# Performance work log

Hardware: AMD Instinct MI355X
Metric: run time of the kernel (lower is better)

The kernel has to match this reference:

```python
import jax, jax.numpy as jnp
import numpy as np

N, K, E = 50000, 32, 50000 * 32
IN_DIM, FEAT_DIM, HID_DIM, OUT_DIM = 128, 64, 64, 32
EPS = 1e-12  # F.normalize eps


def setup_inputs() -> dict:
    key = jax.random.key(0)
    ks = jax.random.split(key, 16)
    s = 0.1  # small init scale (stand-in for xavier)
    return {
        "feat": jax.random.normal(ks[0], (N, IN_DIM), jnp.float32),
        "dists_max": jax.random.uniform(ks[1], (N, K), jnp.float32),
        "src": jax.random.randint(ks[2], (E,), 0, N, jnp.int32),
        "dst": jax.random.randint(ks[3], (E,), 0, N, jnp.int32),
        "w_pre": jax.random.normal(ks[4], (FEAT_DIM, IN_DIM), jnp.float32) * s,
        "b_pre": jnp.zeros((FEAT_DIM,), jnp.float32),
        "Wu1": jax.random.normal(ks[5], (HID_DIM, FEAT_DIM), jnp.float32) * s,
        "bu1": jnp.zeros((HID_DIM,), jnp.float32),
        "Wv1": jax.random.normal(ks[6], (HID_DIM, FEAT_DIM), jnp.float32) * s,
        "bv1": jnp.zeros((HID_DIM,), jnp.float32),
        "wp1": jax.random.normal(ks[7], (1, HID_DIM), jnp.float32) * s,
        "bp1": jnp.zeros((1,), jnp.float32),
        "Wu2": jax.random.normal(ks[8], (OUT_DIM, HID_DIM), jnp.float32) * s,
        "bu2": jnp.zeros((OUT_DIM,), jnp.float32),
        "Wv2": jax.random.normal(ks[9], (OUT_DIM, HID_DIM), jnp.float32) * s,
        "bv2": jnp.zeros((OUT_DIM,), jnp.float32),
        "wp2": jax.random.normal(ks[10], (1, OUT_DIM), jnp.float32) * s,
        "bp2": jnp.zeros((1,), jnp.float32),
    }


def _pgnn_layer(x, sp_dist, src, dst, Wu, bu, Wv, bv, wp, bp, n, k):
    # x: [N, Din]; sp_dist: [E]; src/dst: [E] (anchor edges, E = N*K)
    u = x @ Wu.T + bu  # [N, D]
    v = x @ Wv.T + bv  # [N, D]
    # u_mul_e then v_add_e: message = v_feat[dst] + u_feat[src] * sp_dist
    msg = v[dst] + u[src] * sp_dist[:, None]          # [E, D]
    msg = jax.nn.relu(msg).reshape(n, k, -1)          # [N, K, D]
    out_position = (msg @ wp.T + bp)[..., 0]          # [N, K]
    out_structure = jnp.mean(msg, axis=1)             # [N, D]
    return out_position, out_structure


def reference(feat, dists_max, src, dst, w_pre, b_pre,
              Wu1, bu1, Wv1, bv1, wp1, bp1,
              Wu2, bu2, Wv2, bv2, wp2, bp2):
    n, k = dists_max.shape
    sp_dist = dists_max.reshape(-1)  # anchor_eid == arange(E): edata sp_dist
    x = feat @ w_pre.T + b_pre  # linear_pre (feature_pre=True)
    _, x = _pgnn_layer(x, sp_dist, src, dst, Wu1, bu1, Wv1, bv1, wp1, bp1, n, k)
    # dropout is identity in eval mode
    x_position, _ = _pgnn_layer(x, sp_dist, src, dst, Wu2, bu2, Wv2, bv2, wp2, bp2, n, k)
    # F.normalize(p=2, dim=-1)
    norm = jnp.maximum(jnp.linalg.norm(x_position, axis=-1, keepdims=True), EPS)
    return x_position / norm
```

## Files before the change

### kernel.cpp

```cpp
#include <hip/hip_runtime.h>

constexpr int NN = 50000;
constexpr int KANCH = 32;

typedef __attribute__((ext_vector_type(8))) short bfrag;
typedef __attribute__((ext_vector_type(4))) float ffrag;

static __device__ __forceinline__ float bf2f(unsigned short u) {
    return __uint_as_float(((unsigned int)u) << 16);
}
static __device__ __forceinline__ unsigned short f2bf(float f) {
    unsigned int x = __float_as_uint(f);
    x += 0x7FFFu + ((x >> 16) & 1u);
    return (unsigned short)(x >> 16);
}

__global__ __launch_bounds__(256) void k_prep(
    const float* __restrict__ w_pre, const float* __restrict__ b_pre,
    const float* __restrict__ Wu1, const float* __restrict__ bu1,
    const float* __restrict__ Wv1, const float* __restrict__ bv1,
    unsigned short* __restrict__ wcat1, float* __restrict__ bias1)
{
    int gid = blockIdx.x * 256 + threadIdx.x;
    if (gid < 16384) {
        int j = gid >> 7, i = gid & 127;
        const float* Wr = (j < 64) ? (Wu1 + j * 64) : (Wv1 + (j - 64) * 64);
        float a = 0.f;
        for (int t = 0; t < 64; ++t) a += Wr[t] * w_pre[t * 128 + i];
        wcat1[gid] = f2bf(a);
    } else if (gid < 16384 + 128) {
        int j = gid - 16384;
        const float* Wr = (j < 64) ? (Wu1 + j * 64) : (Wv1 + (j - 64) * 64);
        float a = (j < 64) ? bu1[j] : bv1[j - 64];
        for (int t = 0; t < 64; ++t) a += Wr[t] * b_pre[t];
        bias1[j] = a;
    }
}

__global__ __launch_bounds__(256) void k_gemm1(
    const float* __restrict__ feat,
    const unsigned short* __restrict__ wcat,
    const float* __restrict__ bias,
    unsigned short* __restrict__ ub,
    unsigned short* __restrict__ vb,
    int nTiles)
{
    __shared__ unsigned short s_w[128 * 136];
    __shared__ float s_b[128];
    int tid = threadIdx.x;
    for (int idx = tid; idx < 128 * 16; idx += 256) {
        int r = idx >> 4, c8 = idx & 15;
        const uint4* g = reinterpret_cast<const uint4*>(wcat + r * 128 + c8 * 8);
        *reinterpret_cast<uint4*>(&s_w[r * 136 + c8 * 8]) = *g;
    }
    if (tid < 128) s_b[tid] = bias[tid];
    __syncthreads();

    int wv = __builtin_amdgcn_readfirstlane(tid >> 6);
    int lane = tid & 63;
    int col = lane & 15;
    int grp = lane >> 4;
    int slot = blockIdx.x * 4 + wv;
    int stride = gridDim.x * 4;
    for (int tile = slot; tile < nTiles; tile += stride) {
        int n0 = tile * 16;
        const float* fp = feat + (size_t)(n0 + col) * 128 + grp * 8;
        bfrag AH[4], AL[4];
#pragma unroll
        for (int s = 0; s < 4; ++s) {
            float4 p0 = *reinterpret_cast<const float4*>(fp + s * 32);
            float4 p1 = *reinterpret_cast<const float4*>(fp + s * 32 + 4);
            float a8[8] = {p0.x, p0.y, p0.z, p0.w, p1.x, p1.y, p1.z, p1.w};
#pragma unroll
            for (int e = 0; e < 8; ++e) {
                unsigned short hb = f2bf(a8[e]);
                AH[s][e] = (short)hb;
                AL[s][e] = (short)f2bf(a8[e] - bf2f(hb));
            }
        }
#pragma unroll
        for (int t = 0; t < 8; ++t) {
            ffrag a = {0.f, 0.f, 0.f, 0.f};
#pragma unroll
            for (int s = 0; s < 4; ++s) {
                const bfrag w = *reinterpret_cast<const bfrag*>(
                    &s_w[(t * 16 + col) * 136 + s * 32 + grp * 8]);
                a = __builtin_amdgcn_mfma_f32_16x16x32_bf16(AH[s], w, a, 0, 0, 0);
                a = __builtin_amdgcn_mfma_f32_16x16x32_bf16(AL[s], w, a, 0, 0, 0);
            }
            float bb = s_b[t * 16 + col];
#pragma unroll
            for (int j = 0; j < 4; ++j) {
                int node = n0 + grp * 4 + j;
                unsigned short o = f2bf(a[j] + bb);
                if (t < 4) ub[(size_t)node * 64 + t * 16 + col] = o;
                else       vb[(size_t)node * 64 + (t - 4) * 16 + col] = o;
            }
        }
    }
}

__global__ __launch_bounds__(256) void k_fuse(
    const ushort4* __restrict__ u1v, const ushort4* __restrict__ v1v,
    const int* __restrict__ src, const int* __restrict__ dst,
    const float* __restrict__ dists,
    const float* __restrict__ Wu2, const float* __restrict__ bu2,
    const float* __restrict__ Wv2, const float* __restrict__ bv2,
    unsigned short* __restrict__ u2b,
    unsigned short* __restrict__ v2b)
{
    __shared__ float s_x2[4 * 64];
    int tid = threadIdx.x;
    int wv = __builtin_amdgcn_readfirstlane(tid >> 6);
    int lane = tid & 63;
    const float* wrow = (lane < 32) ? (Wu2 + lane * 64) : (Wv2 + (lane - 32) * 64);
    float wcol[64];
#pragma unroll
    for (int i4 = 0; i4 < 16; ++i4) {
        float4 t = *reinterpret_cast<const float4*>(wrow + i4 * 4);
        wcol[i4 * 4 + 0] = t.x; wcol[i4 * 4 + 1] = t.y;
        wcol[i4 * 4 + 2] = t.z; wcol[i4 * 4 + 3] = t.w;
    }
    float bj = (lane < 32) ? bu2[lane] : bv2[lane - 32];

    int c = lane & 15;
    int es = lane >> 4;
    int slot = blockIdx.x * 4 + wv;
    int stride = gridDim.x * 4;
    float* sx = &s_x2[wv * 64];
    for (int n = slot; n < NN; n += stride) {
        int base = n * KANCH;
        float a0 = 0.f, a1 = 0.f, a2 = 0.f, a3 = 0.f;
#pragma unroll 4
        for (int kk = 0; kk < 8; ++kk) {
            int k = kk * 4 + es;
            int sk = src[base + k];
            int dk = dst[base + k];
            float sp = dists[base + k];
            ushort4 uu = u1v[(size_t)sk * 16 + c];
            ushort4 vv = v1v[(size_t)dk * 16 + c];
            a0 += fmaxf(fmaf(bf2f(uu.x), sp, bf2f(vv.x)), 0.f);
            a1 += fmaxf(fmaf(bf2f(uu.y), sp, bf2f(vv.y)), 0.f);
            a2 += fmaxf(fmaf(bf2f(uu.z), sp, bf2f(vv.z)), 0.f);
            a3 += fmaxf(fmaf(bf2f(uu.w), sp, bf2f(vv.w)), 0.f);
        }
        a0 += __shfl_xor(a0, 16); a0 += __shfl_xor(a0, 32);
        a1 += __shfl_xor(a1, 16); a1 += __shfl_xor(a1, 32);
        a2 += __shfl_xor(a2, 16); a2 += __shfl_xor(a2, 32);
        a3 += __shfl_xor(a3, 16); a3 += __shfl_xor(a3, 32);
        if (lane < 16) {
            float4 r;
            r.x = a0 * 0.03125f; r.y = a1 * 0.03125f;
            r.z = a2 * 0.03125f; r.w = a3 * 0.03125f;
            *reinterpret_cast<float4*>(sx + c * 4) = r;
        }
        float acc = bj;
#pragma unroll
        for (int i = 0; i < 64; ++i)
            acc = fmaf(sx[i], wcol[i], acc);
        unsigned short o = f2bf(acc);
        if (lane < 32) u2b[(size_t)n * 32 + lane] = o;
        else           v2b[(size_t)n * 32 + (lane - 32)] = o;
    }
}

__global__ __launch_bounds__(256, 4) void k_out(
    const ushort4* __restrict__ u2v, const ushort4* __restrict__ v2v,
    const int* __restrict__ src, const int* __restrict__ dst,
    const float* __restrict__ dists, const float* __restrict__ wp2,
    const float* __restrict__ bp2, float* __restrict__ out)
{
    int tid = threadIdx.x;
    int wv = __builtin_amdgcn_readfirstlane(tid >> 6);
    int lane = tid & 63;
    int c = lane & 7;
    int es = lane >> 3;
    int slot = blockIdx.x * 4 + wv;
    int stride = gridDim.x * 4;
    float4 w4 = reinterpret_cast<const float4*>(wp2)[c];
    float bp = bp2[0];
    const int nPairs = NN / 2;
    for (int p = slot; p < nPairs; p += stride) {
        int nA = p * 2, nB = nA + 1;
        int baseA = nA * KANCH, baseB = nB * KANCH;
        int4   sA = *reinterpret_cast<const int4*>(src + baseA + es * 4);
        int4   dA = *reinterpret_cast<const int4*>(dst + baseA + es * 4);
        float4 pA = *reinterpret_cast<const float4*>(dists + baseA + es * 4);
        int4   sB = *reinterpret_cast<const int4*>(src + baseB + es * 4);
        int4   dB = *reinterpret_cast<const int4*>(dst + baseB + es * 4);
        float4 pB = *reinterpret_cast<const float4*>(dists + baseB + es * 4);
        ushort4 uA[4], vA[4], uB[4], vB[4];
        uA[0] = u2v[(size_t)sA.x * 8 + c]; uA[1] = u2v[(size_t)sA.y * 8 + c];
        uA[2] = u2v[(size_t)sA.z * 8 + c]; uA[3] = u2v[(size_t)sA.w * 8 + c];
        vA[0] = v2v[(size_t)dA.x * 8 + c]; vA[1] = v2v[(size_t)dA.y * 8 + c];
        vA[2] = v2v[(size_t)dA.z * 8 + c]; vA[3] = v2v[(size_t)dA.w * 8 + c];
        uB[0] = u2v[(size_t)sB.x * 8 + c]; uB[1] = u2v[(size_t)sB.y * 8 + c];
        uB[2] = u2v[(size_t)sB.z * 8 + c]; uB[3] = u2v[(size_t)sB.w * 8 + c];
        vB[0] = v2v[(size_t)dB.x * 8 + c]; vB[1] = v2v[(size_t)dB.y * 8 + c];
        vB[2] = v2v[(size_t)dB.z * 8 + c]; vB[3] = v2v[(size_t)dB.w * 8 + c];
        float spA[4] = {pA.x, pA.y, pA.z, pA.w};
        float spB[4] = {pB.x, pB.y, pB.z, pB.w};
        float qA[4], qB[4];
#pragma unroll
        for (int kk = 0; kk < 4; ++kk) {
            float pa, pb;
            pa  = fmaxf(fmaf(bf2f(uA[kk].x), spA[kk], bf2f(vA[kk].x)), 0.f) * w4.x;
            pa += fmaxf(fmaf(bf2f(uA[kk].y), spA[kk], bf2f(vA[kk].y)), 0.f) * w4.y;
            pa += fmaxf(fmaf(bf2f(uA[kk].z), spA[kk], bf2f(vA[kk].z)), 0.f) * w4.z;
            pa += fmaxf(fmaf(bf2f(uA[kk].w), spA[kk], bf2f(vA[kk].w)), 0.f) * w4.w;
            pb  = fmaxf(fmaf(bf2f(uB[kk].x), spB[kk], bf2f(vB[kk].x)), 0.f) * w4.x;
            pb += fmaxf(fmaf(bf2f(uB[kk].y), spB[kk], bf2f(vB[kk].y)), 0.f) * w4.y;
            pb += fmaxf(fmaf(bf2f(uB[kk].z), spB[kk], bf2f(vB[kk].z)), 0.f) * w4.z;
            pb += fmaxf(fmaf(bf2f(uB[kk].w), spB[kk], bf2f(vB[kk].w)), 0.f) * w4.w;
            pa += __shfl_xor(pa, 1); pa += __shfl_xor(pa, 2); pa += __shfl_xor(pa, 4);
            pb += __shfl_xor(pb, 1); pb += __shfl_xor(pb, 2); pb += __shfl_xor(pb, 4);
            qA[kk] = pa; qB[kk] = pb;
        }
        int t = lane & 31;
        int srcl = (t >> 2) * 8;
        float cA0 = __shfl(qA[0], srcl), cA1 = __shfl(qA[1], srcl);
        float cA2 = __shfl(qA[2], srcl), cA3 = __shfl(qA[3], srcl);
        float cB0 = __shfl(qB[0], srcl), cB1 = __shfl(qB[1], srcl);
        float cB2 = __shfl(qB[2], srcl), cB3 = __shfl(qB[3], srcl);
        int ks = t & 3;
        float qa = (ks == 0) ? cA0 : (ks == 1) ? cA1 : (ks == 2) ? cA2 : cA3;
        float qb = (ks == 0) ? cB0 : (ks == 1) ? cB1 : (ks == 2) ? cB2 : cB3;
        float q = ((lane < 32) ? qa : qb) + bp;
        float ss = q * q;
#pragma unroll
        for (int off = 16; off >= 1; off >>= 1)
            ss += __shfl_xor(ss, off);
        float den = fmaxf(sqrtf(ss), 1e-12f);
        float o = q / den;
        if (lane < 32) out[(size_t)nA * KANCH + t] = o;
        else           out[(size_t)nB * KANCH + t] = o;
    }
}

extern "C" void kernel_launch(void* const* d_in, const int* in_sizes, int n_in,
                              void* d_out, int out_size, void* d_ws, size_t ws_size,
                              hipStream_t stream)
{
    const float* feat  = (const float*)d_in[0];
    const float* dists = (const float*)d_in[1];
    const int*   src   = (const int*)d_in[2];
    const int*   dst   = (const int*)d_in[3];
    const float* w_pre = (const float*)d_in[4];
    const float* b_pre = (const float*)d_in[5];
    const float* Wu1   = (const float*)d_in[6];
    const float* bu1   = (const float*)d_in[7];
    const float* Wv1   = (const float*)d_in[8];
    const float* bv1   = (const float*)d_in[9];
    const float* Wu2   = (const float*)d_in[12];
    const float* bu2   = (const float*)d_in[13];
    const float* Wv2   = (const float*)d_in[14];
    const float* bv2   = (const float*)d_in[15];
    const float* wp2   = (const float*)d_in[16];
    const float* bp2   = (const float*)d_in[17];
    float* out = (float*)d_out;

    unsigned short* wcat1 = (unsigned short*)d_ws;
    float* bias1 = (float*)(wcat1 + 16384);
    unsigned short* u1b = (unsigned short*)(bias1 + 128);
    unsigned short* v1b = u1b + (size_t)NN * 64;
    unsigned short* u2b = v1b + (size_t)NN * 64;
    unsigned short* v2b = u2b + (size_t)NN * 32;

    k_prep<<<65, 256, 0, stream>>>(w_pre, b_pre, Wu1, bu1, Wv1, bv1,
                                   wcat1, bias1);
    k_gemm1<<<782, 256, 0, stream>>>(feat, wcat1, bias1, u1b, v1b, NN / 16);
    k_fuse<<<2048, 256, 0, stream>>>((const ushort4*)u1b, (const ushort4*)v1b,
                                     src, dst, dists,
                                     Wu2, bu2, Wv2, bv2, u2b, v2b);
    k_out<<<2048, 256, 0, stream>>>((const ushort4*)u2b, (const ushort4*)v2b,
                                    src, dst, dists, wp2, bp2, out);
}
```

Baseline: 117.6 us.

## Batch layer-2 projection over 8 nodes with bf16 MFMA in fused gather kernel

The fused gather kernel now handles batches of 8 nodes per wave. It stores the mean-aggregated features as bf16 in shared memory and computes the 64->64 layer-2 projection with 16x16x32 bf16 MFMA, using a bf16 weight matrix prepared in k_prep. This replaces the per-lane 64-register weight column and the scalar FMA dot product. Index and distance loads are vectorized so each lane issues 8 gathers at once, which raises memory-level parallelism. The cost is extra bf16 rounding of the aggregated features and half of the MFMA output rows going unused.

```diff
diff --git a/kernel.cpp b/kernel.cpp
--- a/kernel.cpp
+++ b/kernel.cpp
@@ -19,7 +19,9 @@
     const float* __restrict__ w_pre, const float* __restrict__ b_pre,
     const float* __restrict__ Wu1, const float* __restrict__ bu1,
     const float* __restrict__ Wv1, const float* __restrict__ bv1,
-    unsigned short* __restrict__ wcat1, float* __restrict__ bias1)
+    const float* __restrict__ Wu2, const float* __restrict__ Wv2,
+    unsigned short* __restrict__ wcat1, float* __restrict__ bias1,
+    unsigned short* __restrict__ wcat2)
 {
     int gid = blockIdx.x * 256 + threadIdx.x;
     if (gid < 16384) {
@@ -28,8 +30,13 @@
         float a = 0.f;
         for (int t = 0; t < 64; ++t) a += Wr[t] * w_pre[t * 128 + i];
         wcat1[gid] = f2bf(a);
-    } else if (gid < 16384 + 128) {
-        int j = gid - 16384;
+    } else if (gid < 16384 + 4096) {
+        int g = gid - 16384;
+        int j = g >> 6, i = g & 63;
+        float w = (j < 32) ? Wu2[j * 64 + i] : Wv2[(j - 32) * 64 + i];
+        wcat2[g] = f2bf(w);
+    } else if (gid < 16384 + 4096 + 128) {
+        int j = gid - (16384 + 4096);
         const float* Wr = (j < 64) ? (Wu1 + j * 64) : (Wv1 + (j - 64) * 64);
         float a = (j < 64) ? bu1[j] : bv1[j - 64];
         for (int t = 0; t < 64; ++t) a += Wr[t] * b_pre[t];
@@ -100,67 +107,104 @@
     }
 }
 
-__global__ __launch_bounds__(256) void k_fuse(
+__global__ __launch_bounds__(256) void k_fuse2(
     const ushort4* __restrict__ u1v, const ushort4* __restrict__ v1v,
     const int* __restrict__ src, const int* __restrict__ dst,
     const float* __restrict__ dists,
-    const float* __restrict__ Wu2, const float* __restrict__ bu2,
-    const float* __restrict__ Wv2, const float* __restrict__ bv2,
+    const unsigned short* __restrict__ wcat2,
+    const float* __restrict__ bu2, const float* __restrict__ bv2,
     unsigned short* __restrict__ u2b,
     unsigned short* __restrict__ v2b)
 {
-    __shared__ float s_x2[4 * 64];
+    __shared__ unsigned short s_x2[4][16 * 72];
     int tid = threadIdx.x;
     int wv = __builtin_amdgcn_readfirstlane(tid >> 6);
     int lane = tid & 63;
-    const float* wrow = (lane < 32) ? (Wu2 + lane * 64) : (Wv2 + (lane - 32) * 64);
-    float wcol[64];
-#pragma unroll
-    for (int i4 = 0; i4 < 16; ++i4) {
-        float4 t = *reinterpret_cast<const float4*>(wrow + i4 * 4);
-        wcol[i4 * 4 + 0] = t.x; wcol[i4 * 4 + 1] = t.y;
-        wcol[i4 * 4 + 2] = t.z; wcol[i4 * 4 + 3] = t.w;
-    }
-    float bj = (lane < 32) ? bu2[lane] : bv2[lane - 32];
-
     int c = lane & 15;
     int es = lane >> 4;
+    bfrag Bf[4][2];
+#pragma unroll
+    for (int t = 0; t < 4; ++t)
+#pragma unroll
+        for (int s = 0; s < 2; ++s) {
+            uint4 raw = *reinterpret_cast<const uint4*>(
+                wcat2 + (t * 16 + c) * 64 + s * 32 + es * 8);
+            Bf[t][s] = *reinterpret_cast<const bfrag*>(&raw);
+        }
+    float bb[4];
+#pragma unroll
+    for (int t = 0; t < 4; ++t)
+        bb[t] = (t < 2) ? bu2[t * 16 + c] : bv2[(t - 2) * 16 + c];
+
+    unsigned short* sx = &s_x2[wv][0];
     int slot = blockIdx.x * 4 + wv;
     int stride = gridDim.x * 4;
-    float* sx = &s_x2[wv * 64];
-    for (int n = slot; n < NN; n += stride) {
-        int base = n * KANCH;
-        float a0 = 0.f, a1 = 0.f, a2 = 0.f, a3 = 0.f;
-#pragma unroll 4
-        for (int kk = 0; kk < 8; ++kk) {
-            int k = kk * 4 + es;
-            int sk = src[base + k];
-            int dk = dst[base + k];
-            float sp = dists[base + k];
-            ushort4 uu = u1v[(size_t)sk * 16 + c];
-            ushort4 vv = v1v[(size_t)dk * 16 + c];
-            a0 += fmaxf(fmaf(bf2f(uu.x), sp, bf2f(vv.x)), 0.f);
-            a1 += fmaxf(fmaf(bf2f(uu.y), sp, bf2f(vv.y)), 0.f);
-            a2 += fmaxf(fmaf(bf2f(uu.z), sp, bf2f(vv.z)), 0.f);
-            a3 += fmaxf(fmaf(bf2f(uu.w), sp, bf2f(vv.w)), 0.f);
-        }
-        a0 += __shfl_xor(a0, 16); a0 += __shfl_xor(a0, 32);
-        a1 += __shfl_xor(a1, 16); a1 += __shfl_xor(a1, 32);
-        a2 += __shfl_xor(a2, 16); a2 += __shfl_xor(a2, 32);
-        a3 += __shfl_xor(a3, 16); a3 += __shfl_xor(a3, 32);
-        if (lane < 16) {
-            float4 r;
-            r.x = a0 * 0.03125f; r.y = a1 * 0.03125f;
-            r.z = a2 * 0.03125f; r.w = a3 * 0.03125f;
-            *reinterpret_cast<float4*>(sx + c * 4) = r;
-        }
-        float acc = bj;
-#pragma unroll
-        for (int i = 0; i < 64; ++i)
-            acc = fmaf(sx[i], wcol[i], acc);
-        unsigned short o = f2bf(acc);
-        if (lane < 32) u2b[(size_t)n * 32 + lane] = o;
-        else           v2b[(size_t)n * 32 + (lane - 32)] = o;
+    const int nBatch = NN / 8;
+    for (int b = slot; b < nBatch; b += stride) {
+        int n0 = b * 8;
+        for (int i = 0; i < 8; ++i) {
+            int base = (n0 + i) * KANCH + es * 8;
+            int4   si0 = *reinterpret_cast<const int4*>(src + base);
+            int4   si1 = *reinterpret_cast<const int4*>(src + base + 4);
+            int4   di0 = *reinterpret_cast<const int4*>(dst + base);
+            int4   di1 = *reinterpret_cast<const int4*>(dst + base + 4);
+            float4 pp0 = *reinterpret_cast<const float4*>(dists + base);
+            float4 pp1 = *reinterpret_cast<const float4*>(dists + base + 4);
+            ushort4 uu[8], vvv[8];
+            uu[0] = u1v[(size_t)si0.x * 16 + c]; uu[1] = u1v[(size_t)si0.y * 16 + c];
+            uu[2] = u1v[(size_t)si0.z * 16 + c]; uu[3] = u1v[(size_t)si0.w * 16 + c];
+            uu[4] = u1v[(size_t)si1.x * 16 + c]; uu[5] = u1v[(size_t)si1.y * 16 + c];
+            uu[6] = u1v[(size_t)si1.z * 16 + c]; uu[7] = u1v[(size_t)si1.w * 16 + c];
+            vvv[0] = v1v[(size_t)di0.x * 16 + c]; vvv[1] = v1v[(size_t)di0.y * 16 + c];
+            vvv[2] = v1v[(size_t)di0.z * 16 + c]; vvv[3] = v1v[(size_t)di0.w * 16 + c];
+            vvv[4] = v1v[(size_t)di1.x * 16 + c]; vvv[5] = v1v[(size_t)di1.y * 16 + c];
+            vvv[6] = v1v[(size_t)di1.z * 16 + c]; vvv[7] = v1v[(size_t)di1.w * 16 + c];
+            float sp[8] = {pp0.x, pp0.y, pp0.z, pp0.w, pp1.x, pp1.y, pp1.z, pp1.w};
+            float a0 = 0.f, a1 = 0.f, a2 = 0.f, a3 = 0.f;
+#pragma unroll
+            for (int kk = 0; kk < 8; ++kk) {
+                a0 += fmaxf(fmaf(bf2f(uu[kk].x), sp[kk], bf2f(vvv[kk].x)), 0.f);
+                a1 += fmaxf(fmaf(bf2f(uu[kk].y), sp[kk], bf2f(vvv[kk].y)), 0.f);
+                a2 += fmaxf(fmaf(bf2f(uu[kk].z), sp[kk], bf2f(vvv[kk].z)), 0.f);
+                a3 += fmaxf(fmaf(bf2f(uu[kk].w), sp[kk], bf2f(vvv[kk].w)), 0.f);
+            }
+            a0 += __shfl_xor(a0, 16); a0 += __shfl_xor(a0, 32);
+            a1 += __shfl_xor(a1, 16); a1 += __shfl_xor(a1, 32);
+            a2 += __shfl_xor(a2, 16); a2 += __shfl_xor(a2, 32);
+            a3 += __shfl_xor(a3, 16); a3 += __shfl_xor(a3, 32);
+            if (lane < 16) {
+                ushort4 r;
+                r.x = f2bf(a0 * 0.03125f); r.y = f2bf(a1 * 0.03125f);
+                r.z = f2bf(a2 * 0.03125f); r.w = f2bf(a3 * 0.03125f);
+                *reinterpret_cast<ushort4*>(&sx[i * 72 + c * 4]) = r;
+            }
+        }
+        bfrag A[2];
+#pragma unroll
+        for (int s = 0; s < 2; ++s)
+            A[s] = *reinterpret_cast<const bfrag*>(
+                &sx[(lane & 15) * 72 + s * 32 + es * 8]);
+        ffrag acc[4];
+#pragma unroll
+        for (int t = 0; t < 4; ++t) {
+            acc[t] = ffrag{0.f, 0.f, 0.f, 0.f};
+#pragma unroll
+            for (int s = 0; s < 2; ++s)
+                acc[t] = __builtin_amdgcn_mfma_f32_16x16x32_bf16(
+                    A[s], Bf[t][s], acc[t], 0, 0, 0);
+        }
+        if (es < 2) {
+#pragma unroll
+            for (int t = 0; t < 4; ++t) {
+#pragma unroll
+                for (int j = 0; j < 4; ++j) {
+                    int node = n0 + es * 4 + j;
+                    unsigned short o = f2bf(acc[t][j] + bb[t]);
+                    if (t < 2) u2b[(size_t)node * 32 + t * 16 + c] = o;
+                    else       v2b[(size_t)node * 32 + (t - 2) * 16 + c] = o;
+                }
+            }
+        }
     }
 }
 
@@ -261,17 +305,18 @@
 
     unsigned short* wcat1 = (unsigned short*)d_ws;
     float* bias1 = (float*)(wcat1 + 16384);
-    unsigned short* u1b = (unsigned short*)(bias1 + 128);
+    unsigned short* wcat2 = (unsigned short*)(bias1 + 128);
+    unsigned short* u1b = wcat2 + 4096;
     unsigned short* v1b = u1b + (size_t)NN * 64;
     unsigned short* u2b = v1b + (size_t)NN * 64;
     unsigned short* v2b = u2b + (size_t)NN * 32;
 
-    k_prep<<<65, 256, 0, stream>>>(w_pre, b_pre, Wu1, bu1, Wv1, bv1,
-                                   wcat1, bias1);
+    k_prep<<<81, 256, 0, stream>>>(w_pre, b_pre, Wu1, bu1, Wv1, bv1,
+                                   Wu2, Wv2, wcat1, bias1, wcat2);
     k_gemm1<<<782, 256, 0, stream>>>(feat, wcat1, bias1, u1b, v1b, NN / 16);
-    k_fuse<<<2048, 256, 0, stream>>>((const ushort4*)u1b, (const ushort4*)v1b,
-                                     src, dst, dists,
-                                     Wu2, bu2, Wv2, bv2, u2b, v2b);
+    k_fuse2<<<1563, 256, 0, stream>>>((const ushort4*)u1b, (const ushort4*)v1b,
+                                      src, dst, dists, wcat2, bu2, bv2,
+                                      u2b, v2b);
     k_out<<<2048, 256, 0, stream>>>((const ushort4*)u2b, (const ushort4*)v2b,
                                     src, dst, dists, wp2, bp2, out);
 }
```

Result: faster. 110.2 us (-6.3%).
